# Kernel tuning notes

Hardware: AMD Instinct MI355X
Metric: run time of the kernel (lower is better)

## Reference

```python
import jax, jax.numpy as jnp
import numpy as np
from math import ceil, log2

LEVELS = 8
# pywt 'db4' filters (length 8)
DB4_DEC_HI = np.array([-0.23037781330885523, 0.7148465705525415, -0.6308807679295904,
                       -0.02798376941698385, 0.18703481171888114, 0.030841381835986965,
                       -0.032883011666982945, -0.010597401784997278], dtype=np.float32)
DB4_REC_HI = np.array([-0.010597401784997278, -0.032883011666982945, 0.030841381835986965,
                       0.18703481171888114, -0.02798376941698385, -0.6308807679295904,
                       0.7148465705525415, -0.23037781330885523], dtype=np.float32)


def setup_inputs() -> dict:
    key = jax.random.key(0)
    x = jax.random.normal(key, (2048, 3000), dtype=jnp.float32)
    scaling = jnp.tile(jnp.asarray(DB4_DEC_HI), (LEVELS, 1))       # [levels, 8]
    scaling_rec = jnp.tile(jnp.asarray(DB4_REC_HI), (LEVELS, 1))   # [levels, 8]
    return {"input": x, "scaling": scaling, "scaling_rec": scaling_rec}


def _make_wavelet(h):
    # g = flip(h); g[1::2] *= -1
    g = jnp.flip(h, axis=-1)
    signs = jnp.where(jnp.arange(g.shape[-1]) % 2 == 1, -1.0, 1.0).astype(g.dtype)
    return g * signs


def _circ_conv(x, filt, transpose=False):
    # FFT-based circular convolution (filter zero-padded to input length)
    L = x.shape[-1]
    ra = jnp.fft.rfft(x)
    rb = jnp.fft.rfft(filt, n=L)
    if transpose:
        rb = jnp.conj(rb)
    return jnp.fft.irfft(ra * rb, n=L)


def _upsample2(x):
    # interleave zeros: out[:, ::2] = x
    n, k = x.shape
    out = jnp.zeros((n, 2 * k), dtype=x.dtype)
    return out.at[:, ::2].set(x)


def _forward(x, scaling, scaling_rec):
    levels = scaling.shape[0]
    m = x.shape[1]
    L = 2 ** ceil(log2(m))
    p0 = (L - m) // 2
    p1 = ceil((L - m) / 2)
    x = jnp.pad(x, ((0, 0), (p0, p1)), mode="edge")  # ReplicationPad1d

    approx = x
    wav_coeffs = []
    for lvl in range(levels):
        wavelet = _make_wavelet(scaling_rec[lvl])
        details = _circ_conv(approx, wavelet)[:, ::2]
        approx = _circ_conv(approx, scaling[lvl])[:, ::2]
        wav_coeffs.append(details)
    wav_coeffs.append(approx)

    # (no thresholding: the original forward copies coeffs unmodified)
    filtered = list(wav_coeffs)
    approx = filtered[-1]
    for lvl in reversed(range(levels)):
        details = filtered[lvl]
        wav_syn = _make_wavelet(scaling_rec[lvl])
        d_rec = _circ_conv(_upsample2(details), wav_syn, transpose=True)
        a_rec = _circ_conv(_upsample2(approx), scaling[lvl], transpose=True)
        approx = d_rec + a_rec

    recon = approx[:, p0:m + p1]
    coeffs = jnp.concatenate(wav_coeffs, axis=-1)  # total length == L
    return recon, coeffs


def reference(input, scaling, scaling_rec):
    return _forward(input, scaling, scaling_rec)
```

## Files before the change

### kernel.cpp

```cpp
#include <hip/hip_runtime.h>

#define NROWS 2048
#define MLEN  3000
#define LPAD  4096
#define PAD0  548
#define NLVL  8
#define NT    256

union F4 { float4 v; float f[4]; };

__device__ inline void lds_barrier() {
    asm volatile("s_waitcnt lgkmcnt(0)\n\ts_barrier" ::: "memory");
}

__global__ __launch_bounds__(NT, 8) void despawn_kernel(
    const float* __restrict__ x,
    const float* __restrict__ scaling,
    const float* __restrict__ scaling_rec,
    float* __restrict__ recon_out,
    float* __restrict__ coef_out)
{
    __shared__ __align__(16) float SA[2048];
    __shared__ __align__(16) float SB[2112];
    __shared__ __align__(16) float CS[512];

    const int tid = threadIdx.x;
    const int row = blockIdx.x;
    float* const crow = coef_out + (size_t)row * LPAD;
    const float* xr = x + (size_t)row * MLEN;

    {
        const int lag = (blockIdx.x >> 3) & 3;
        for (int i = 0; i < lag; ++i) __builtin_amdgcn_s_sleep(8);
    }

    {
        float S[8], Wr[8];
#pragma unroll
        for (int k = 0; k < 8; ++k) { S[k] = scaling[k]; Wr[k] = scaling_rec[7 - k]; }
#pragma unroll
        for (int h = 0; h < 2; ++h) {
            const int j0 = 1024 * h;
            const int n0 = 2 * j0 + 8 * tid - 8;
            F4 V0, V1, V2, V3;
            if (n0 >= PAD0 && n0 + 15 <= PAD0 + MLEN - 1) {
                const float4* src = reinterpret_cast<const float4*>(xr + (n0 - PAD0));
                V0.v = src[0]; V1.v = src[1]; V2.v = src[2]; V3.v = src[3];
            } else {
                const float x0  = xr[0];
                const float xhi = xr[MLEN - 1];
#pragma unroll
                for (int j = 0; j < 16; ++j) {
                    const int n = n0 + j;
                    const int m = (n < 0) ? n + LPAD : n;
                    float val;
                    if (m < PAD0)             val = x0;
                    else if (m >= PAD0 + MLEN) val = xhi;
                    else                       val = xr[m - PAD0];
                    if (j < 4)       V0.f[j & 3] = val;
                    else if (j < 8)  V1.f[j & 3] = val;
                    else if (j < 12) V2.f[j & 3] = val;
                    else             V3.f[j & 3] = val;
                }
            }
            float e[8] = {V0.f[0],V0.f[2],V1.f[0],V1.f[2],V2.f[0],V2.f[2],V3.f[0],V3.f[2]};
            float o[8] = {V0.f[1],V0.f[3],V1.f[1],V1.f[3],V2.f[1],V2.f[3],V3.f[1],V3.f[3]};
            float ds[4], as[4];
            __builtin_amdgcn_s_setprio(1);
#pragma unroll
            for (int u = 0; u < 4; ++u) {
                float d = 0.f, a = 0.f;
#pragma unroll
                for (int m = 0; m < 4; ++m) {
                    const float vE = e[4 + u - m];
                    const float vO = o[3 + u - m];
                    d = fmaf(vE, Wr[2 * m], d);
                    d = fmaf(vO, -Wr[2 * m + 1], d);
                    a = fmaf(vE, S[2 * m], a);
                    a = fmaf(vO, S[2 * m + 1], a);
                }
                ds[u] = d; as[u] = a;
            }
            __builtin_amdgcn_s_setprio(0);
            F4 dv; dv.f[0] = ds[0]; dv.f[1] = ds[1]; dv.f[2] = ds[2]; dv.f[3] = ds[3];
            reinterpret_cast<float4*>(crow + j0)[tid] = dv.v;
            *reinterpret_cast<float2*>(SA + (j0 >> 1) + 2 * tid)        = make_float2(as[0], as[2]);
            *reinterpret_cast<float2*>(SA + 1024 + (j0 >> 1) + 2 * tid) = make_float2(as[1], as[3]);
        }
    }
    lds_barrier();

    {
        float* cur = SA;
        float* alt = SB;
        int H = 1024;
        int coff = 2048;
        for (int lvl = 1; lvl < NLVL; ++lvl) {
            float S[8], Wr[8];
#pragma unroll
            for (int k = 0; k < 8; ++k) {
                S[k]  = scaling[lvl * 8 + k];
                Wr[k] = scaling_rec[lvl * 8 + 7 - k];
            }
            const int q = H >> 2;
            const int qm = q - 1;
            const float4* ev4 = reinterpret_cast<const float4*>(cur);
            const float4* od4 = reinterpret_cast<const float4*>(cur + H);
            float4* dst4 = reinterpret_cast<float4*>(crow + coff);
            float4* mir4 = (lvl == 1) ? reinterpret_cast<float4*>(&SB[1088])
                         : (lvl == 2) ? reinterpret_cast<float4*>(&SA[512])
                                      : reinterpret_cast<float4*>(&CS[coff - 3584]);
            for (int t = tid; t < q; t += NT) {
                F4 Ea, Eb, Oa, Ob;
                Ea.v = ev4[(t - 1) & qm];
                Eb.v = ev4[t];
                Oa.v = od4[(t - 1) & qm];
                Ob.v = od4[t];
                float e[8] = {Ea.f[0],Ea.f[1],Ea.f[2],Ea.f[3],Eb.f[0],Eb.f[1],Eb.f[2],Eb.f[3]};
                float o[8] = {Oa.f[0],Oa.f[1],Oa.f[2],Oa.f[3],Ob.f[0],Ob.f[1],Ob.f[2],Ob.f[3]};
                float ds[4], as[4];
                __builtin_amdgcn_s_setprio(1);
#pragma unroll
                for (int u = 0; u < 4; ++u) {
                    float d = 0.f, a = 0.f;
#pragma unroll
                    for (int m = 0; m < 4; ++m) {
                        const float vE = e[4 + u - m];
                        const float vO = o[3 + u - m];
                        d = fmaf(vE, Wr[2 * m], d);
                        d = fmaf(vO, -Wr[2 * m + 1], d);
                        a = fmaf(vE, S[2 * m], a);
                        a = fmaf(vO, S[2 * m + 1], a);
                    }
                    ds[u] = d; as[u] = a;
                }
                __builtin_amdgcn_s_setprio(0);
                F4 dv; dv.f[0] = ds[0]; dv.f[1] = ds[1]; dv.f[2] = ds[2]; dv.f[3] = ds[3];
                dst4[t] = dv.v;
                mir4[t] = dv.v;
                if (lvl < NLVL - 1) {
                    *reinterpret_cast<float2*>(alt + 2 * t)            = make_float2(as[0], as[2]);
                    *reinterpret_cast<float2*>(alt + (H >> 1) + 2 * t) = make_float2(as[1], as[3]);
                } else {
                    F4 av; av.f[0] = as[0]; av.f[1] = as[1]; av.f[2] = as[2]; av.f[3] = as[3];
                    *reinterpret_cast<float4*>(&CS[496 + 4 * t])         = av.v;
                    *reinterpret_cast<float4*>(crow + LPAD - 16 + 4 * t) = av.v;
                }
            }
            lds_barrier();
            coff += H;
            float* tmp = cur; cur = alt; alt = tmp;
            H >>= 1;
        }
    }

    __syncthreads();

    const float* a = &CS[496];
    float* obuf = SA;
    int len = 16;
    for (int lvl = NLVL - 1; lvl >= 1; --lvl) {
        float S[8], Wr[8];
#pragma unroll
        for (int k = 0; k < 8; ++k) {
            S[k]  = scaling[lvl * 8 + k];
            Wr[k] = scaling_rec[lvl * 8 + 7 - k];
        }
        const int Mout = len << 1;
        const int doff = LPAD - (LPAD >> lvl);
        const float4* d4 = (lvl >= 3) ? reinterpret_cast<const float4*>(&CS[doff - 3584])
                         : (lvl == 2) ? reinterpret_cast<const float4*>(&SA[512])
                                      : reinterpret_cast<const float4*>(&SB[1088]);
        const float4* a4 = reinterpret_cast<const float4*>(a);
        const int gq = Mout >> 3;
        const int fm = (len >> 2) - 1;
        for (int g = tid; g < gq; g += NT) {
            F4 Da, Db, Aa, Ab;
            Da.v = d4[g]; Db.v = d4[(g + 1) & fm];
            Aa.v = a4[g]; Ab.v = a4[(g + 1) & fm];
            float dd[8] = {Da.f[0],Da.f[1],Da.f[2],Da.f[3],Db.f[0],Db.f[1],Db.f[2],Db.f[3]};
            float aa[8] = {Aa.f[0],Aa.f[1],Aa.f[2],Aa.f[3],Ab.f[0],Ab.f[1],Ab.f[2],Ab.f[3]};
            float out[8];
            __builtin_amdgcn_s_setprio(1);
#pragma unroll
            for (int u = 0; u < 8; ++u) {
                const int p = u & 1, c = (u + 1) >> 1;
                float s = 0.f;
#pragma unroll
                for (int m = 0; m < 4; ++m) {
                    const float w = Wr[p + 2 * m];
                    s = fmaf(dd[c + m], p ? -w : w, s);
                    s = fmaf(aa[c + m], S[p + 2 * m], s);
                }
                out[u] = s;
            }
            __builtin_amdgcn_s_setprio(0);
            F4 o0, o1;
            o0.f[0] = out[0]; o0.f[1] = out[1]; o0.f[2] = out[2]; o0.f[3] = out[3];
            o1.f[0] = out[4]; o1.f[1] = out[5]; o1.f[2] = out[6]; o1.f[3] = out[7];
            float4* ob4 = reinterpret_cast<float4*>(obuf + 8 * g);
            ob4[0] = o0.v; ob4[1] = o1.v;
        }
        lds_barrier();
        a = obuf;
        obuf = (obuf == SA) ? SB : SA;
        len = Mout;
    }

    {
        float S[8], Wr[8];
#pragma unroll
        for (int k = 0; k < 8; ++k) { S[k] = scaling[k]; Wr[k] = scaling_rec[7 - k]; }
        const float4* d4 = reinterpret_cast<const float4*>(crow);
        const float4* a4 = reinterpret_cast<const float4*>(a);
        const int fm = (len >> 2) - 1;
        float* const ro = recon_out + (size_t)row * MLEN;
        for (int g = tid; g < (LPAD >> 3); g += NT) {
            F4 Da, Db, Aa, Ab;
            Da.v = d4[g]; Db.v = d4[(g + 1) & fm];
            Aa.v = a4[g]; Ab.v = a4[(g + 1) & fm];
            float dd[8] = {Da.f[0],Da.f[1],Da.f[2],Da.f[3],Db.f[0],Db.f[1],Db.f[2],Db.f[3]};
            float aa[8] = {Aa.f[0],Aa.f[1],Aa.f[2],Aa.f[3],Ab.f[0],Ab.f[1],Ab.f[2],Ab.f[3]};
            float out[8];
            __builtin_amdgcn_s_setprio(1);
#pragma unroll
            for (int u = 0; u < 8; ++u) {
                const int p = u & 1, c = (u + 1) >> 1;
                float s = 0.f;
#pragma unroll
                for (int m = 0; m < 4; ++m) {
                    const float w = Wr[p + 2 * m];
                    s = fmaf(dd[c + m], p ? -w : w, s);
                    s = fmaf(aa[c + m], S[p + 2 * m], s);
                }
                out[u] = s;
            }
            __builtin_amdgcn_s_setprio(0);
            const int n0 = 8 * g;
            if (n0 >= PAD0 && n0 + 8 <= PAD0 + MLEN) {
                F4 o0, o1;
                o0.f[0] = out[0]; o0.f[1] = out[1]; o0.f[2] = out[2]; o0.f[3] = out[3];
                o1.f[0] = out[4]; o1.f[1] = out[5]; o1.f[2] = out[6]; o1.f[3] = out[7];
                float4* r4 = reinterpret_cast<float4*>(ro + (n0 - PAD0));
                r4[0] = o0.v; r4[1] = o1.v;
            } else {
#pragma unroll
                for (int u = 0; u < 8; ++u) {
                    const int n = n0 + u;
                    if (n >= PAD0 && n < PAD0 + MLEN) ro[n - PAD0] = out[u];
                }
            }
        }
    }
}

extern "C" void kernel_launch(void* const* d_in, const int* in_sizes, int n_in,
                              void* d_out, int out_size, void* d_ws, size_t ws_size,
                              hipStream_t stream) {
    const float* x           = (const float*)d_in[0];
    const float* scaling     = (const float*)d_in[1];
    const float* scaling_rec = (const float*)d_in[2];
    float* recon = (float*)d_out;
    float* coefo = recon + (size_t)NROWS * MLEN;
    despawn_kernel<<<dim3(NROWS), dim3(NT), 0, stream>>>(x, scaling, scaling_rec,
                                                         recon, coefo);
    (void)in_sizes; (void)n_in; (void)out_size; (void)d_ws; (void)ws_size;
}
```

Measured before the change: 95.70 us.

## Use one wavefront per row to drop block barriers, read level-1/2 details from global

Each row is now handled by a single 64-thread wavefront, so the block-wide s_barrier between wavelet levels becomes a plain LDS wait (lgkmcnt) fence. LDS use shrinks because the level-1 and level-2 detail mirrors are dropped. Those details are instead re-read from the just-written global coefficient rows after a vmcnt wait. The last three synthesis levels are unrolled into explicit stages. The setprio hints and the staggered start sleep are removed. In exchange each workgroup does four times more serial work per thread, and correctness relies on the global writes being visible to the same wave after the vmcnt wait.

```diff
diff --git a/kernel.cpp b/kernel.cpp
--- a/kernel.cpp
+++ b/kernel.cpp
@@ -5,43 +5,36 @@
 #define LPAD  4096
 #define PAD0  548
 #define NLVL  8
-#define NT    256
 
 union F4 { float4 v; float f[4]; };
 
-__device__ inline void lds_barrier() {
-    asm volatile("s_waitcnt lgkmcnt(0)\n\ts_barrier" ::: "memory");
+__device__ inline void wave_fence() {
+    asm volatile("s_waitcnt lgkmcnt(0)" ::: "memory");
 }
 
-__global__ __launch_bounds__(NT, 8) void despawn_kernel(
+__global__ __launch_bounds__(64, 2) void despawn_kernel(
     const float* __restrict__ x,
     const float* __restrict__ scaling,
     const float* __restrict__ scaling_rec,
     float* __restrict__ recon_out,
     float* __restrict__ coef_out)
 {
-    __shared__ __align__(16) float SA[2048];
-    __shared__ __align__(16) float SB[2112];
+    __shared__ __align__(16) float A[2048];
+    __shared__ __align__(16) float B[1024];
     __shared__ __align__(16) float CS[512];
 
-    const int tid = threadIdx.x;
+    const int t   = threadIdx.x;
     const int row = blockIdx.x;
     float* const crow = coef_out + (size_t)row * LPAD;
     const float* xr = x + (size_t)row * MLEN;
 
     {
-        const int lag = (blockIdx.x >> 3) & 3;
-        for (int i = 0; i < lag; ++i) __builtin_amdgcn_s_sleep(8);
-    }
-
-    {
         float S[8], Wr[8];
 #pragma unroll
         for (int k = 0; k < 8; ++k) { S[k] = scaling[k]; Wr[k] = scaling_rec[7 - k]; }
-#pragma unroll
-        for (int h = 0; h < 2; ++h) {
-            const int j0 = 1024 * h;
-            const int n0 = 2 * j0 + 8 * tid - 8;
+        for (int it = 0; it < 8; ++it) {
+            const int g  = t + (it << 6);
+            const int n0 = (g << 3) - 8;
             F4 V0, V1, V2, V3;
             if (n0 >= PAD0 && n0 + 15 <= PAD0 + MLEN - 1) {
                 const float4* src = reinterpret_cast<const float4*>(xr + (n0 - PAD0));
@@ -54,7 +47,7 @@
                     const int n = n0 + j;
                     const int m = (n < 0) ? n + LPAD : n;
                     float val;
-                    if (m < PAD0)             val = x0;
+                    if (m < PAD0)              val = x0;
                     else if (m >= PAD0 + MLEN) val = xhi;
                     else                       val = xr[m - PAD0];
                     if (j < 4)       V0.f[j & 3] = val;
@@ -66,7 +59,6 @@
             float e[8] = {V0.f[0],V0.f[2],V1.f[0],V1.f[2],V2.f[0],V2.f[2],V3.f[0],V3.f[2]};
             float o[8] = {V0.f[1],V0.f[3],V1.f[1],V1.f[3],V2.f[1],V2.f[3],V3.f[1],V3.f[3]};
             float ds[4], as[4];
-            __builtin_amdgcn_s_setprio(1);
 #pragma unroll
             for (int u = 0; u < 4; ++u) {
                 float d = 0.f, a = 0.f;
@@ -81,18 +73,17 @@
                 }
                 ds[u] = d; as[u] = a;
             }
-            __builtin_amdgcn_s_setprio(0);
             F4 dv; dv.f[0] = ds[0]; dv.f[1] = ds[1]; dv.f[2] = ds[2]; dv.f[3] = ds[3];
-            reinterpret_cast<float4*>(crow + j0)[tid] = dv.v;
-            *reinterpret_cast<float2*>(SA + (j0 >> 1) + 2 * tid)        = make_float2(as[0], as[2]);
-            *reinterpret_cast<float2*>(SA + 1024 + (j0 >> 1) + 2 * tid) = make_float2(as[1], as[3]);
-        }
-    }
-    lds_barrier();
-
-    {
-        float* cur = SA;
-        float* alt = SB;
+            reinterpret_cast<float4*>(crow)[g] = dv.v;
+            *reinterpret_cast<float2*>(A + 2 * g)        = make_float2(as[0], as[2]);
+            *reinterpret_cast<float2*>(A + 1024 + 2 * g) = make_float2(as[1], as[3]);
+        }
+    }
+    wave_fence();
+
+    {
+        float* cur = A;
+        float* alt = B;
         int H = 1024;
         int coff = 2048;
         for (int lvl = 1; lvl < NLVL; ++lvl) {
@@ -107,19 +98,16 @@
             const float4* ev4 = reinterpret_cast<const float4*>(cur);
             const float4* od4 = reinterpret_cast<const float4*>(cur + H);
             float4* dst4 = reinterpret_cast<float4*>(crow + coff);
-            float4* mir4 = (lvl == 1) ? reinterpret_cast<float4*>(&SB[1088])
-                         : (lvl == 2) ? reinterpret_cast<float4*>(&SA[512])
-                                      : reinterpret_cast<float4*>(&CS[coff - 3584]);
-            for (int t = tid; t < q; t += NT) {
+            float4* mir4 = reinterpret_cast<float4*>(CS + (coff - 3584));
+            for (int g = t; g < q; g += 64) {
                 F4 Ea, Eb, Oa, Ob;
-                Ea.v = ev4[(t - 1) & qm];
-                Eb.v = ev4[t];
-                Oa.v = od4[(t - 1) & qm];
-                Ob.v = od4[t];
+                Ea.v = ev4[(g - 1) & qm];
+                Eb.v = ev4[g];
+                Oa.v = od4[(g - 1) & qm];
+                Ob.v = od4[g];
                 float e[8] = {Ea.f[0],Ea.f[1],Ea.f[2],Ea.f[3],Eb.f[0],Eb.f[1],Eb.f[2],Eb.f[3]};
                 float o[8] = {Oa.f[0],Oa.f[1],Oa.f[2],Oa.f[3],Ob.f[0],Ob.f[1],Ob.f[2],Ob.f[3]};
                 float ds[4], as[4];
-                __builtin_amdgcn_s_setprio(1);
 #pragma unroll
                 for (int u = 0; u < 4; ++u) {
                     float d = 0.f, a = 0.f;
@@ -134,32 +122,29 @@
                     }
                     ds[u] = d; as[u] = a;
                 }
-                __builtin_amdgcn_s_setprio(0);
                 F4 dv; dv.f[0] = ds[0]; dv.f[1] = ds[1]; dv.f[2] = ds[2]; dv.f[3] = ds[3];
-                dst4[t] = dv.v;
-                mir4[t] = dv.v;
+                dst4[g] = dv.v;
+                if (lvl >= 3) mir4[g] = dv.v;
                 if (lvl < NLVL - 1) {
-                    *reinterpret_cast<float2*>(alt + 2 * t)            = make_float2(as[0], as[2]);
-                    *reinterpret_cast<float2*>(alt + (H >> 1) + 2 * t) = make_float2(as[1], as[3]);
+                    *reinterpret_cast<float2*>(alt + 2 * g)            = make_float2(as[0], as[2]);
+                    *reinterpret_cast<float2*>(alt + (H >> 1) + 2 * g) = make_float2(as[1], as[3]);
                 } else {
                     F4 av; av.f[0] = as[0]; av.f[1] = as[1]; av.f[2] = as[2]; av.f[3] = as[3];
-                    *reinterpret_cast<float4*>(&CS[496 + 4 * t])         = av.v;
-                    *reinterpret_cast<float4*>(crow + LPAD - 16 + 4 * t) = av.v;
-                }
-            }
-            lds_barrier();
+                    *reinterpret_cast<float4*>(CS + 496 + 4 * g)          = av.v;
+                    *reinterpret_cast<float4*>(crow + LPAD - 16 + 4 * g)  = av.v;
+                }
+            }
+            wave_fence();
             coff += H;
             float* tmp = cur; cur = alt; alt = tmp;
             H >>= 1;
         }
     }
 
-    __syncthreads();
-
-    const float* a = &CS[496];
-    float* obuf = SA;
+    const float* a = CS + 496;
+    float* obuf = A;
     int len = 16;
-    for (int lvl = NLVL - 1; lvl >= 1; --lvl) {
+    for (int lvl = NLVL - 1; lvl >= 3; --lvl) {
         float S[8], Wr[8];
 #pragma unroll
         for (int k = 0; k < 8; ++k) {
@@ -168,20 +153,17 @@
         }
         const int Mout = len << 1;
         const int doff = LPAD - (LPAD >> lvl);
-        const float4* d4 = (lvl >= 3) ? reinterpret_cast<const float4*>(&CS[doff - 3584])
-                         : (lvl == 2) ? reinterpret_cast<const float4*>(&SA[512])
-                                      : reinterpret_cast<const float4*>(&SB[1088]);
+        const float4* d4 = reinterpret_cast<const float4*>(CS + (doff - 3584));
         const float4* a4 = reinterpret_cast<const float4*>(a);
         const int gq = Mout >> 3;
         const int fm = (len >> 2) - 1;
-        for (int g = tid; g < gq; g += NT) {
+        for (int g = t; g < gq; g += 64) {
             F4 Da, Db, Aa, Ab;
             Da.v = d4[g]; Db.v = d4[(g + 1) & fm];
             Aa.v = a4[g]; Ab.v = a4[(g + 1) & fm];
             float dd[8] = {Da.f[0],Da.f[1],Da.f[2],Da.f[3],Db.f[0],Db.f[1],Db.f[2],Db.f[3]};
             float aa[8] = {Aa.f[0],Aa.f[1],Aa.f[2],Aa.f[3],Ab.f[0],Ab.f[1],Ab.f[2],Ab.f[3]};
             float out[8];
-            __builtin_amdgcn_s_setprio(1);
 #pragma unroll
             for (int u = 0; u < 8; ++u) {
                 const int p = u & 1, c = (u + 1) >> 1;
@@ -194,35 +176,37 @@
                 }
                 out[u] = s;
             }
-            __builtin_amdgcn_s_setprio(0);
             F4 o0, o1;
             o0.f[0] = out[0]; o0.f[1] = out[1]; o0.f[2] = out[2]; o0.f[3] = out[3];
             o1.f[0] = out[4]; o1.f[1] = out[5]; o1.f[2] = out[6]; o1.f[3] = out[7];
             float4* ob4 = reinterpret_cast<float4*>(obuf + 8 * g);
             ob4[0] = o0.v; ob4[1] = o1.v;
         }
-        lds_barrier();
+        wave_fence();
         a = obuf;
-        obuf = (obuf == SA) ? SB : SA;
+        obuf = (obuf == A) ? B : A;
         len = Mout;
     }
 
-    {
-        float S[8], Wr[8];
-#pragma unroll
-        for (int k = 0; k < 8; ++k) { S[k] = scaling[k]; Wr[k] = scaling_rec[7 - k]; }
-        const float4* d4 = reinterpret_cast<const float4*>(crow);
+    asm volatile("s_waitcnt vmcnt(0)" ::: "memory");
+
+    {
+        float S[8], Wr[8];
+#pragma unroll
+        for (int k = 0; k < 8; ++k) {
+            S[k]  = scaling[2 * 8 + k];
+            Wr[k] = scaling_rec[2 * 8 + 7 - k];
+        }
+        const float4* d4 = reinterpret_cast<const float4*>(crow + 3072);
         const float4* a4 = reinterpret_cast<const float4*>(a);
-        const int fm = (len >> 2) - 1;
-        float* const ro = recon_out + (size_t)row * MLEN;
-        for (int g = tid; g < (LPAD >> 3); g += NT) {
+        const int fm = 127;
+        for (int g = t; g < 128; g += 64) {
             F4 Da, Db, Aa, Ab;
             Da.v = d4[g]; Db.v = d4[(g + 1) & fm];
             Aa.v = a4[g]; Ab.v = a4[(g + 1) & fm];
             float dd[8] = {Da.f[0],Da.f[1],Da.f[2],Da.f[3],Db.f[0],Db.f[1],Db.f[2],Db.f[3]};
             float aa[8] = {Aa.f[0],Aa.f[1],Aa.f[2],Aa.f[3],Ab.f[0],Ab.f[1],Ab.f[2],Ab.f[3]};
             float out[8];
-            __builtin_amdgcn_s_setprio(1);
 #pragma unroll
             for (int u = 0; u < 8; ++u) {
                 const int p = u & 1, c = (u + 1) >> 1;
@@ -235,7 +219,80 @@
                 }
                 out[u] = s;
             }
-            __builtin_amdgcn_s_setprio(0);
+            F4 o0, o1;
+            o0.f[0] = out[0]; o0.f[1] = out[1]; o0.f[2] = out[2]; o0.f[3] = out[3];
+            o1.f[0] = out[4]; o1.f[1] = out[5]; o1.f[2] = out[6]; o1.f[3] = out[7];
+            float4* ob4 = reinterpret_cast<float4*>(B + 8 * g);
+            ob4[0] = o0.v; ob4[1] = o1.v;
+        }
+    }
+    wave_fence();
+
+    {
+        float S[8], Wr[8];
+#pragma unroll
+        for (int k = 0; k < 8; ++k) {
+            S[k]  = scaling[1 * 8 + k];
+            Wr[k] = scaling_rec[1 * 8 + 7 - k];
+        }
+        const float4* d4 = reinterpret_cast<const float4*>(crow + 2048);
+        const float4* a4 = reinterpret_cast<const float4*>(B);
+        const int fm = 255;
+        for (int g = t; g < 256; g += 64) {
+            F4 Da, Db, Aa, Ab;
+            Da.v = d4[g]; Db.v = d4[(g + 1) & fm];
+            Aa.v = a4[g]; Ab.v = a4[(g + 1) & fm];
+            float dd[8] = {Da.f[0],Da.f[1],Da.f[2],Da.f[3],Db.f[0],Db.f[1],Db.f[2],Db.f[3]};
+            float aa[8] = {Aa.f[0],Aa.f[1],Aa.f[2],Aa.f[3],Ab.f[0],Ab.f[1],Ab.f[2],Ab.f[3]};
+            float out[8];
+#pragma unroll
+            for (int u = 0; u < 8; ++u) {
+                const int p = u & 1, c = (u + 1) >> 1;
+                float s = 0.f;
+#pragma unroll
+                for (int m = 0; m < 4; ++m) {
+                    const float w = Wr[p + 2 * m];
+                    s = fmaf(dd[c + m], p ? -w : w, s);
+                    s = fmaf(aa[c + m], S[p + 2 * m], s);
+                }
+                out[u] = s;
+            }
+            F4 o0, o1;
+            o0.f[0] = out[0]; o0.f[1] = out[1]; o0.f[2] = out[2]; o0.f[3] = out[3];
+            o1.f[0] = out[4]; o1.f[1] = out[5]; o1.f[2] = out[6]; o1.f[3] = out[7];
+            float4* ob4 = reinterpret_cast<float4*>(A + 8 * g);
+            ob4[0] = o0.v; ob4[1] = o1.v;
+        }
+    }
+    wave_fence();
+
+    {
+        float S[8], Wr[8];
+#pragma unroll
+        for (int k = 0; k < 8; ++k) { S[k] = scaling[k]; Wr[k] = scaling_rec[7 - k]; }
+        const float4* d4 = reinterpret_cast<const float4*>(crow);
+        const float4* a4 = reinterpret_cast<const float4*>(A);
+        const int fm = 511;
+        float* const ro = recon_out + (size_t)row * MLEN;
+        for (int g = t; g < (LPAD >> 3); g += 64) {
+            F4 Da, Db, Aa, Ab;
+            Da.v = d4[g]; Db.v = d4[(g + 1) & fm];
+            Aa.v = a4[g]; Ab.v = a4[(g + 1) & fm];
+            float dd[8] = {Da.f[0],Da.f[1],Da.f[2],Da.f[3],Db.f[0],Db.f[1],Db.f[2],Db.f[3]};
+            float aa[8] = {Aa.f[0],Aa.f[1],Aa.f[2],Aa.f[3],Ab.f[0],Ab.f[1],Ab.f[2],Ab.f[3]};
+            float out[8];
+#pragma unroll
+            for (int u = 0; u < 8; ++u) {
+                const int p = u & 1, c = (u + 1) >> 1;
+                float s = 0.f;
+#pragma unroll
+                for (int m = 0; m < 4; ++m) {
+                    const float w = Wr[p + 2 * m];
+                    s = fmaf(dd[c + m], p ? -w : w, s);
+                    s = fmaf(aa[c + m], S[p + 2 * m], s);
+                }
+                out[u] = s;
+            }
             const int n0 = 8 * g;
             if (n0 >= PAD0 && n0 + 8 <= PAD0 + MLEN) {
                 F4 o0, o1;
@@ -262,7 +319,7 @@
     const float* scaling_rec = (const float*)d_in[2];
     float* recon = (float*)d_out;
     float* coefo = recon + (size_t)NROWS * MLEN;
-    despawn_kernel<<<dim3(NROWS), dim3(NT), 0, stream>>>(x, scaling, scaling_rec,
+    despawn_kernel<<<dim3(NROWS), dim3(64), 0, stream>>>(x, scaling, scaling_rec,
                                                          recon, coefo);
     (void)in_sizes; (void)n_in; (void)out_size; (void)d_ws; (void)ws_size;
 }
```

After: 104.1 us. 8.8% more time.
